# Performance work log

Hardware: AMD Instinct MI355X
Metric: run time of the kernel (lower is better)

The kernel has to match this reference:

```python
import jax, jax.numpy as jnp
import numpy as np

B, Z_DIM, T_DIM, ACT_E, CF, N_ACT, STEPS = 256, 256, 512, 256, 1024, 64, 64


def setup_inputs() -> dict:
    key = jax.random.key(0)
    ks = jax.random.split(key, 12)
    s = 0.02
    def n(k, shape):
        return jax.random.normal(k, shape, jnp.float32) * s
    return {
        "z": jax.random.normal(ks[0], (B, Z_DIM), jnp.float32),
        "W_z2t": n(ks[1], (T_DIM, Z_DIM)), "b_z2t": jnp.zeros((T_DIM,), jnp.float32),
        "E": n(ks[2], (N_ACT, ACT_E)),  # encoder_act2e embedding table
        "Wih_a": n(ks[3], (4 * CF, T_DIM + ACT_E)), "Whh_a": n(ks[4], (4 * CF, CF)),
        "bih_a": jnp.zeros((4 * CF,), jnp.float32), "bhh_a": jnp.zeros((4 * CF,), jnp.float32),
        "Wih_t": n(ks[5], (4 * CF, T_DIM + ACT_E + 1)), "Whh_t": n(ks[6], (4 * CF, CF)),
        "bih_t": jnp.zeros((4 * CF,), jnp.float32), "bhh_t": jnp.zeros((4 * CF,), jnp.float32),
        "W_act": n(ks[7], (N_ACT, CF)), "b_act": jnp.zeros((N_ACT,), jnp.float32),
        "W_ts1": n(ks[8], (CF // 2, CF)), "b_ts1": jnp.zeros((CF // 2,), jnp.float32),
        "W_ts2": n(ks[9], (1, CF // 2)), "b_ts2": jnp.zeros((1,), jnp.float32),
    }


def _lstm_step(x, h, c, Wih, Whh, bih, bhh):
    # PyTorch LSTM gate order: i, f, g, o
    gates = x @ Wih.T + h @ Whh.T + bih + bhh
    i, f, g, o = jnp.split(gates, 4, axis=-1)
    c = jax.nn.sigmoid(f) * c + jax.nn.sigmoid(i) * jnp.tanh(g)
    h = jax.nn.sigmoid(o) * jnp.tanh(c)
    return h, c


def reference(z, W_z2t, b_z2t, E, Wih_a, Whh_a, bih_a, bhh_a,
              Wih_t, Whh_t, bih_t, bhh_t, W_act, b_act,
              W_ts1, b_ts1, W_ts2, b_ts2):
    Bz = z.shape[0]
    t_rec = jax.nn.relu(z @ W_z2t.T + b_z2t)                 # [B, t_dim]
    zeros_h = jnp.zeros((Bz, CF), z.dtype)
    act_emb0 = jnp.broadcast_to(E[-1], (Bz, ACT_E))          # EOT token embedding
    ts0 = jnp.zeros((Bz, 1), z.dtype)

    def step(carry, _):
        h_a, c_a, h_t, c_t, act_emb, ts = carry
        x_a = jnp.concatenate([t_rec, act_emb], axis=1)       # [B, t_dim+act_e]
        h_a, c_a = _lstm_step(x_a, h_a, c_a, Wih_a, Whh_a, bih_a, bhh_a)
        logits = h_a @ W_act.T + b_act                        # [B, num_activities]
        act_emb = E[jnp.argmax(logits, axis=1)]               # [B, act_e]
        x_t = jnp.concatenate([t_rec, act_emb, ts], axis=1)   # [B, t_dim+act_e+1]
        h_t, c_t = _lstm_step(x_t, h_t, c_t, Wih_t, Whh_t, bih_t, bhh_t)
        ts = jax.nn.relu(h_t @ W_ts1.T + b_ts1) @ W_ts2.T + b_ts2  # [B, 1]
        return (h_a, c_a, h_t, c_t, act_emb, ts), (logits, ts)

    carry0 = (zeros_h, zeros_h, zeros_h, zeros_h, act_emb0, ts0)
    _, (logits_seq, ts_seq) = jax.lax.scan(step, carry0, None, length=STEPS)
    acts_rec = jax.nn.softmax(jnp.transpose(logits_seq, (1, 0, 2)), axis=2)  # [B, T, A]
    ts_rec = jnp.transpose(ts_seq[..., 0], (1, 0))                            # [B, T]
    return acts_rec, ts_rec
```

## Files before the change

### kernel.cpp

```cpp
#include <hip/hip_runtime.h>
#include <stdint.h>

typedef unsigned int u32;
typedef float  f32x4 __attribute__((ext_vector_type(4)));
typedef float  f32x2 __attribute__((ext_vector_type(2)));
typedef double f64x2 __attribute__((ext_vector_type(2)));
typedef double f64x4 __attribute__((ext_vector_type(4)));

constexpr int NT = 256;
constexpr int BB = 256;
constexpr int ZD = 256;
constexpr int TD = 512;
constexpr int CF = 1024;
constexpr int G4 = 4096;
constexpr int NA = 64;
constexpr int NSTEP = 64;
constexpr int TS_OFF = BB * NSTEP * NA;

constexpr int RSF = 34;

struct P {
  const float *z, *W_z2t, *b_z2t, *E, *Wih_a, *Whh_a, *bih_a, *bhh_a,
              *Wih_t, *Whh_t, *bih_t, *bhh_t, *W_act, *b_act, *W_ts1, *b_ts1, *W_ts2, *b_ts2;
  float* out;
  double *t_rec64, *pre_a64, *E_proj_a64, *h_a64, *c_a64, *gacc_a;
  float *t_rec32, *pre_t, *E_proj_t, *colt, *h_t, *c_t, *gacc_t, *ts_accum;
  int* idxb;
};

__device__ __forceinline__ float sigf(float x){ return 1.f / (1.f + expf(-x)); }
__device__ __forceinline__ float tanhf_(float x){
  float ax = fabsf(x); float e = expf(-2.f * ax);
  float t = 1.f - 2.f * e / (1.f + e);
  return x < 0.f ? -t : t;
}
__device__ __forceinline__ double sigd(double x){ return 1.0 / (1.0 + exp(-x)); }

__global__ void __launch_bounds__(NT) k_setup(P p){
  __shared__ double sz[ZD];
  const int bid = blockIdx.x, tid = threadIdx.x;
  for (int i = tid; i < ZD; i += NT) sz[i] = (double)p.z[bid * ZD + i];
  __syncthreads();
  for (int k = tid; k < TD; k += NT){
    const float* wr = p.W_z2t + (size_t)k * ZD;
    double a = 0.0;
    for (int j = 0; j < ZD; ++j) a = fma((double)wr[j], sz[j], a);
    a += (double)p.b_z2t[k];
    double t = a > 0.0 ? a : 0.0;
    p.t_rec64[(size_t)bid * TD + k] = t;
    p.t_rec32[(size_t)bid * TD + k] = (float)t;
  }
  for (int i = tid; i < CF; i += NT){
    p.c_a64[(size_t)bid * CF + i] = 0.0;
    p.h_a64[(size_t)bid * CF + i] = 0.0;
    p.c_t[(size_t)bid * CF + i] = 0.f;
    p.h_t[(size_t)bid * CF + i] = 0.f;
  }
  if (tid == 0){ p.idxb[bid] = NA - 1; p.ts_accum[bid] = 0.f; }
}

__global__ void __launch_bounds__(NT) k_eproj(P p){
  __shared__ double sz[ZD];
  const int bid = blockIdx.x, tid = threadIdx.x;
  if (bid < 256){
    const int erow = bid >> 2, cchunk = bid & 3;
    for (int i = tid; i < ZD; i += NT) sz[i] = (double)p.E[erow * ZD + i];
    __syncthreads();
    for (int ci = 0; ci < 4; ++ci){
      const int c = cchunk * 1024 + ci * 256 + tid;
      const float* wr = p.Wih_a + (size_t)c * 768 + 512;
      double a = 0.0;
      for (int j = 0; j < 256; ++j) a = fma((double)wr[j], sz[j], a);
      p.E_proj_a64[(size_t)erow * G4 + c] = a;
    }
  } else if (bid < 512){
    const int erow = (bid - 256) >> 2, cchunk = (bid - 256) & 3;
    for (int i = tid; i < ZD; i += NT) sz[i] = (double)p.E[erow * ZD + i];
    __syncthreads();
    for (int ci = 0; ci < 4; ++ci){
      const int c = cchunk * 1024 + ci * 256 + tid;
      const float* wr = p.Wih_t + (size_t)c * 769 + 512;
      float a = 0.f;
      for (int j = 0; j < 256; ++j) a = fmaf(wr[j], (float)sz[j], a);
      p.E_proj_t[(size_t)erow * G4 + c] = a;
    }
  } else {
    const int c = (bid - 512) * 256 + tid;
    p.colt[c] = p.Wih_t[(size_t)c * 769 + 768];
  }
}

template <bool A64, bool OUT64, bool BIAS>
__device__ void mgemm64(char* smem, const void* __restrict__ Av, int lda,
                        const float* __restrict__ B, int ldb,
                        int rowb, int colb, int K,
                        const void* __restrict__ addin,
                        const float* __restrict__ bih, const float* __restrict__ bhh,
                        void* __restrict__ outv){
  double* As = (double*)smem;
  double* Bs = As + 64 * RSF;
  const int tid = threadIdx.x;
  const int lane = tid & 63;
  const int wm = (tid >> 7) & 1, wn = (tid >> 6) & 1;
  const int m = lane & 15, q = lane >> 4;
  const int tr = tid >> 2, tkq = tid & 3;
  const double* A64p = (const double*)Av;
  const float*  A32p = (const float*)Av;

  double av[8], bv[8];
  auto loadchunk = [&](int kb){
    if (A64){
      const double* ap = A64p + (size_t)(rowb + tr) * lda + kb + tkq * 8;
      #pragma unroll
      for (int j = 0; j < 8; ++j) av[j] = ap[j];
    } else {
      const float* ap = A32p + (size_t)(rowb + tr) * lda + kb + tkq * 8;
      #pragma unroll
      for (int j = 0; j < 8; ++j) av[j] = (double)ap[j];
    }
    const float* bp = B + (size_t)(colb + tr) * ldb + kb + tkq * 8;
    #pragma unroll
    for (int j = 0; j < 8; ++j) bv[j] = (double)bp[j];
  };
  f64x4 acc[2][2];
  #pragma unroll
  for (int g = 0; g < 2; ++g)
    #pragma unroll
    for (int h = 0; h < 2; ++h) acc[g][h] = f64x4{0.0,0.0,0.0,0.0};

  loadchunk(0);
  for (int kb = 0; kb < K; kb += 32){
    __syncthreads();
    {
      double* arow = As + tr * RSF + tkq * 8;
      double* brow = Bs + tr * RSF + tkq * 8;
      #pragma unroll
      for (int j = 0; j < 4; ++j){
        *(f64x2*)(arow + j * 2) = f64x2{av[j], av[j + 4]};
        *(f64x2*)(brow + j * 2) = f64x2{bv[j], bv[j + 4]};
      }
    }
    __syncthreads();
    if (kb + 32 < K) loadchunk(kb + 32);
    #pragma unroll
    for (int sp = 0; sp < 4; ++sp){
      const f64x2 a0 = *(const f64x2*)(As + (wm * 32 +  0 + m) * RSF + sp * 8 + q * 2);
      const f64x2 a1 = *(const f64x2*)(As + (wm * 32 + 16 + m) * RSF + sp * 8 + q * 2);
      const f64x2 b0 = *(const f64x2*)(Bs + (wn * 32 +  0 + m) * RSF + sp * 8 + q * 2);
      const f64x2 b1 = *(const f64x2*)(Bs + (wn * 32 + 16 + m) * RSF + sp * 8 + q * 2);
      acc[0][0] = __builtin_amdgcn_mfma_f64_16x16x4f64(a0[0], b0[0], acc[0][0], 0, 0, 0);
      acc[0][1] = __builtin_amdgcn_mfma_f64_16x16x4f64(a0[0], b1[0], acc[0][1], 0, 0, 0);
      acc[1][0] = __builtin_amdgcn_mfma_f64_16x16x4f64(a1[0], b0[0], acc[1][0], 0, 0, 0);
      acc[1][1] = __builtin_amdgcn_mfma_f64_16x16x4f64(a1[0], b1[0], acc[1][1], 0, 0, 0);
      acc[0][0] = __builtin_amdgcn_mfma_f64_16x16x4f64(a0[1], b0[1], acc[0][0], 0, 0, 0);
      acc[0][1] = __builtin_amdgcn_mfma_f64_16x16x4f64(a0[1], b1[1], acc[0][1], 0, 0, 0);
      acc[1][0] = __builtin_amdgcn_mfma_f64_16x16x4f64(a1[1], b0[1], acc[1][0], 0, 0, 0);
      acc[1][1] = __builtin_amdgcn_mfma_f64_16x16x4f64(a1[1], b1[1], acc[1][1], 0, 0, 0);
    }
  }
  #pragma unroll
  for (int g = 0; g < 2; ++g){
    const int rb = rowb + wm * 32 + g * 16 + q;
    #pragma unroll
    for (int h = 0; h < 2; ++h){
      const int cc = colb + wn * 32 + h * 16 + m;
      if (BIAS){
        const double bb = (double)bih[cc] + (double)bhh[cc];
        #pragma unroll
        for (int v = 0; v < 4; ++v){
          if (OUT64) ((double*)outv)[(size_t)(rb + 4 * v) * G4 + cc] = acc[g][h][v] + bb;
          else       ((float*) outv)[(size_t)(rb + 4 * v) * G4 + cc] = (float)(acc[g][h][v] + bb);
        }
      } else {
        #pragma unroll
        for (int v = 0; v < 4; ++v){
          const size_t o = (size_t)(rb + 4 * v) * G4 + cc;
          if (OUT64) ((double*)outv)[o] = acc[g][h][v] + ((const double*)addin)[o];
          else       ((float*) outv)[o] = (float)(acc[g][h][v] + (double)((const float*)addin)[o]);
        }
      }
    }
  }
}

__device__ void tshead_j(const P& p, int bid, int hbuf){
  const int tid = threadIdx.x;
  const int tm = bid >> 6, tjq = bid & 63;
  const int rowb = tm * 32;
  const int rt = tid >> 3, j8 = tid & 7;
  const int j = tjq * 8 + j8;
  const float* __restrict__ hr = p.h_t + (size_t)hbuf * BB * CF + (size_t)(rowb + rt) * CF;
  const float* __restrict__ wr = p.W_ts1 + (size_t)j * CF;
  float a0=0,a1=0,a2=0,a3=0;
  for (int k = 0; k < CF; k += 16){
    f32x4 h0 = *(const f32x4*)(hr + k),     h1 = *(const f32x4*)(hr + k + 4);
    f32x4 h2 = *(const f32x4*)(hr + k + 8), h3 = *(const f32x4*)(hr + k + 12);
    f32x4 w0 = *(const f32x4*)(wr + k),     w1 = *(const f32x4*)(wr + k + 4);
    f32x4 w2 = *(const f32x4*)(wr + k + 8), w3 = *(const f32x4*)(wr + k + 12);
    a0 = fmaf(h0[0],w0[0], fmaf(h0[1],w0[1], fmaf(h0[2],w0[2], fmaf(h0[3],w0[3], a0))));
    a1 = fmaf(h1[0],w1[0], fmaf(h1[1],w1[1], fmaf(h1[2],w1[2], fmaf(h1[3],w1[3], a1))));
    a2 = fmaf(h2[0],w2[0], fmaf(h2[1],w2[1], fmaf(h2[2],w2[2], fmaf(h2[3],w2[3], a2))));
    a3 = fmaf(h3[0],w3[0], fmaf(h3[1],w3[1], fmaf(h3[2],w3[2], fmaf(h3[3],w3[3], a3))));
  }
  float v = ((a0 + a1) + (a2 + a3)) + p.b_ts1[j];
  v = (v > 0.f ? v : 0.f) * p.W_ts2[j];
  v += __shfl_xor(v, 1, 64);
  v += __shfl_xor(v, 2, 64);
  v += __shfl_xor(v, 4, 64);
  if (j8 == 0) atomicAdd(p.ts_accum + rowb + rt, v);
}

__global__ void __launch_bounds__(NT) k_pre(P p){
  __shared__ __align__(16) char smem[34816];
  const int bid = blockIdx.x;
  const int hsel = bid >> 8, sub = bid & 255;
  const int rowb = (sub >> 6) * 64, colb = (sub & 63) * 64;
  if (hsel == 0)
    mgemm64<true, true, true>(smem, p.t_rec64, TD, p.Wih_a, 768, rowb, colb, TD,
                              nullptr, p.bih_a, p.bhh_a, p.pre_a64);
  else
    mgemm64<false, false, true>(smem, p.t_rec32, TD, p.Wih_t, 769, rowb, colb, TD,
                                nullptr, p.bih_t, p.bhh_t, p.pre_t);
}

__global__ void __launch_bounds__(NT) k_stepA(P p, int s){
  __shared__ __align__(16) char smem[34816];
  const int bid = blockIdx.x;
  if (s > 0) tshead_j(p, bid, s & 1);
  const int hsel = bid >> 8, sub = bid & 255;
  const int rowb = (sub >> 6) * 64, colb = (sub & 63) * 64;
  const int rd = s & 1;
  if (hsel == 0)
    mgemm64<true, true, false>(smem, p.h_a64 + (size_t)rd * BB * CF, CF, p.Whh_a, CF,
                               rowb, colb, CF, p.pre_a64, nullptr, nullptr, p.gacc_a);
  else
    mgemm64<false, false, false>(smem, p.h_t + (size_t)rd * BB * CF, CF, p.Whh_t, CF,
                                 rowb, colb, CF, p.pre_t, nullptr, nullptr, p.gacc_t);
}

__global__ void __launch_bounds__(NT) k_stepB(P p, int s){
  __shared__ double shd[1092];
  const int b = blockIdx.x, tid = threadIdx.x;
  const int cur = (s + 1) & 1;
  int idxp = p.idxb[b];
  idxp = idxp < 0 ? 0 : (idxp > 63 ? 63 : idxp);
  {
    const double* ga = p.gacc_a + (size_t)b * G4;
    const double* ea = p.E_proj_a64 + (size_t)idxp * G4;
    const int c0 = tid * 4;
    #pragma unroll
    for (int jj = 0; jj < 4; ++jj){
      const int c = c0 + jj;
      double gi = ga[0*CF + c] + ea[0*CF + c];
      double gf = ga[1*CF + c] + ea[1*CF + c];
      double gg = ga[2*CF + c] + ea[2*CF + c];
      double go = ga[3*CF + c] + ea[3*CF + c];
      double cv = p.c_a64[(size_t)b * CF + c];
      double cn = sigd(gf) * cv + sigd(gi) * tanh(gg);
      double hn = sigd(go) * tanh(cn);
      p.c_a64[(size_t)b * CF + c] = cn;
      p.h_a64[(size_t)cur * BB * CF + (size_t)b * CF + c] = hn;
      shd[c] = hn;
    }
  }
  if (tid == 0) shd[1088] = (s == 0) ? 0.0 : ((double)p.ts_accum[b] + (double)p.b_ts2[0]);
  __syncthreads();
  {
    const int w = tid >> 6, l = tid & 63, l15 = l & 15, quad = l >> 4;
    const int a = w * 16 + l15;
    const float* wr = p.W_act + (size_t)a * CF + quad * 256;
    const double* hp = shd + quad * 256;
    double acc = 0.0;
    for (int kk = 0; kk < 256; kk += 4){
      acc = fma((double)wr[kk+0], hp[kk+0], acc);
      acc = fma((double)wr[kk+1], hp[kk+1], acc);
      acc = fma((double)wr[kk+2], hp[kk+2], acc);
      acc = fma((double)wr[kk+3], hp[kk+3], acc);
    }
    acc += __shfl_xor(acc, 16, 64);
    acc += __shfl_xor(acc, 32, 64);
    if (quad == 0) shd[1024 + a] = acc;
  }
  __syncthreads();
  if (tid < 64){
    double acc = shd[1024 + tid] + (double)p.b_act[tid];
    double m = acc;
    #pragma unroll
    for (int off = 32; off; off >>= 1) m = fmax(m, __shfl_xor(m, off, 64));
    unsigned long long ball = __ballot(acc == m);
    int idxv = __ffsll(ball) - 1;
    idxv = idxv < 0 ? 0 : (idxv > 63 ? 63 : idxv);
    double e = exp(acc - m);
    double ssum = e;
    #pragma unroll
    for (int off = 32; off; off >>= 1) ssum += __shfl_xor(ssum, off, 64);
    p.out[(size_t)b * (NSTEP * NA) + s * NA + tid] = (float)(e / ssum);
    if (tid == 0){
      p.idxb[b] = idxv;
      shd[1089] = (double)idxv;
      if (s > 0) p.out[TS_OFF + b * NSTEP + (s - 1)] = (float)shd[1088];
    }
  }
  __syncthreads();
  const float ts_val = (float)shd[1088];
  const int idxv = (int)shd[1089];
  const int c0 = tid * 4;
  const float* gb = p.gacc_t   + (size_t)b * G4;
  const float* eb = p.E_proj_t + (size_t)idxv * G4;
  f32x4 gi = *(const f32x4*)(gb + 0*CF + c0) + *(const f32x4*)(eb + 0*CF + c0) + ts_val * *(const f32x4*)(p.colt + 0*CF + c0);
  f32x4 gf = *(const f32x4*)(gb + 1*CF + c0) + *(const f32x4*)(eb + 1*CF + c0) + ts_val * *(const f32x4*)(p.colt + 1*CF + c0);
  f32x4 gg = *(const f32x4*)(gb + 2*CF + c0) + *(const f32x4*)(eb + 2*CF + c0) + ts_val * *(const f32x4*)(p.colt + 2*CF + c0);
  f32x4 go = *(const f32x4*)(gb + 3*CF + c0) + *(const f32x4*)(eb + 3*CF + c0) + ts_val * *(const f32x4*)(p.colt + 3*CF + c0);
  f32x4 cv = *(f32x4*)(p.c_t + (size_t)b * CF + c0);
  f32x4 cn, hn;
  #pragma unroll
  for (int jj = 0; jj < 4; ++jj){
    float cj = sigf(gf[jj]) * cv[jj] + sigf(gi[jj]) * tanhf_(gg[jj]);
    float hj = sigf(go[jj]) * tanhf_(cj);
    cn[jj] = cj; hn[jj] = hj;
  }
  *(f32x4*)(p.c_t + (size_t)b * CF + c0) = cn;
  *(f32x4*)(p.h_t + (size_t)cur * BB * CF + (size_t)b * CF + c0) = hn;
  __syncthreads();
  if (tid == 0) p.ts_accum[b] = 0.f;
}

__global__ void __launch_bounds__(NT) k_tsfin(P p){
  tshead_j(p, blockIdx.x, 0);
}
__global__ void __launch_bounds__(NT) k_tswrite(P p){
  p.out[TS_OFF + threadIdx.x * NSTEP + 63] = p.ts_accum[threadIdx.x] + p.b_ts2[0];
}

extern "C" void kernel_launch(void* const* d_in, const int* in_sizes, int n_in,
                              void* d_out, int out_size, void* d_ws, size_t ws_size,
                              hipStream_t stream){
  (void)in_sizes; (void)n_in; (void)out_size; (void)ws_size;
  P p;
  p.z     = (const float*)d_in[0];  p.W_z2t = (const float*)d_in[1];  p.b_z2t = (const float*)d_in[2];
  p.E     = (const float*)d_in[3];  p.Wih_a = (const float*)d_in[4];  p.Whh_a = (const float*)d_in[5];
  p.bih_a = (const float*)d_in[6];  p.bhh_a = (const float*)d_in[7];  p.Wih_t = (const float*)d_in[8];
  p.Whh_t = (const float*)d_in[9];  p.bih_t = (const float*)d_in[10]; p.bhh_t = (const float*)d_in[11];
  p.W_act = (const float*)d_in[12]; p.b_act = (const float*)d_in[13]; p.W_ts1 = (const float*)d_in[14];
  p.b_ts1 = (const float*)d_in[15]; p.W_ts2 = (const float*)d_in[16]; p.b_ts2 = (const float*)d_in[17];
  p.out = (float*)d_out;
  char* w = (char*)d_ws;
  size_t off = 0;
  auto alloc = [&](size_t bytes) -> void* { void* r = w + off; off += (bytes + 255) & ~(size_t)255; return r; };
  p.t_rec64    = (double*)alloc((size_t)BB * TD * 8);
  p.pre_a64    = (double*)alloc((size_t)BB * G4 * 8);
  p.E_proj_a64 = (double*)alloc((size_t)NA * G4 * 8);
  p.h_a64      = (double*)alloc((size_t)2 * BB * CF * 8);
  p.c_a64      = (double*)alloc((size_t)BB * CF * 8);
  p.gacc_a     = (double*)alloc((size_t)BB * G4 * 8);
  p.t_rec32    = (float*)alloc((size_t)BB * TD * 4);
  p.pre_t      = (float*)alloc((size_t)BB * G4 * 4);
  p.E_proj_t   = (float*)alloc((size_t)NA * G4 * 4);
  p.colt       = (float*)alloc((size_t)G4 * 4);
  p.h_t        = (float*)alloc((size_t)2 * BB * CF * 4);
  p.c_t        = (float*)alloc((size_t)BB * CF * 4);
  p.gacc_t     = (float*)alloc((size_t)BB * G4 * 4);
  p.ts_accum   = (float*)alloc((size_t)BB * 4);
  p.idxb       = (int*)  alloc((size_t)BB * 4);

  k_setup<<<dim3(256), dim3(NT), 0, stream>>>(p);
  k_eproj<<<dim3(528), dim3(NT), 0, stream>>>(p);
  k_pre  <<<dim3(512), dim3(NT), 0, stream>>>(p);
  for (int s = 0; s < NSTEP; ++s){
    k_stepA<<<dim3(512), dim3(NT), 0, stream>>>(p, s);
    k_stepB<<<dim3(256), dim3(NT), 0, stream>>>(p, s);
  }
  k_tsfin  <<<dim3(512), dim3(NT), 0, stream>>>(p);
  k_tswrite<<<dim3(1),   dim3(NT), 0, stream>>>(p);
}
```

Before: 11.73 ms.

## Double-buffer LDS tiles in f64 MFMA GEMM and stage B operand as fp32

The GEMM mainloop now uses two LDS buffers, so the next chunk can be staged while the current one is consumed. This needs only one barrier per K-chunk instead of two. The B operand is kept as fp32 in LDS and widened to double right before each MFMA, which halves its LDS footprint and store traffic. Row paddings change to odd strides (35 doubles, 33 floats) to spread accesses across LDS banks. Total LDS per block grows, which may cut the number of resident blocks per CU. The odd A stride also leaves the vector LDS accesses only 8-byte aligned.

```diff
diff --git a/kernel.cpp b/kernel.cpp
--- a/kernel.cpp
+++ b/kernel.cpp
@@ -17,7 +17,12 @@
 constexpr int NSTEP = 64;
 constexpr int TS_OFF = BB * NSTEP * NA;
 
-constexpr int RSF = 34;
+constexpr int RSA  = 35;
+constexpr int RBD  = 33;
+constexpr int ATILE = 64 * RSA * 8;
+constexpr int BTILE = 64 * RBD * 4;
+constexpr int BUFB  = ATILE + BTILE;
+constexpr int SMEMB = 2 * BUFB;
 
 struct P {
   const float *z, *W_z2t, *b_z2t, *E, *Wih_a, *Whh_a, *bih_a, *bhh_a,
@@ -97,8 +102,6 @@
                         const void* __restrict__ addin,
                         const float* __restrict__ bih, const float* __restrict__ bhh,
                         void* __restrict__ outv){
-  double* As = (double*)smem;
-  double* Bs = As + 64 * RSF;
   const int tid = threadIdx.x;
   const int lane = tid & 63;
   const int wm = (tid >> 7) & 1, wn = (tid >> 6) & 1;
@@ -107,7 +110,7 @@
   const double* A64p = (const double*)Av;
   const float*  A32p = (const float*)Av;
 
-  double av[8], bv[8];
+  double av[8]; float bvf[8];
   auto loadchunk = [&](int kb){
     if (A64){
       const double* ap = A64p + (size_t)(rowb + tr) * lda + kb + tkq * 8;
@@ -120,8 +123,18 @@
     }
     const float* bp = B + (size_t)(colb + tr) * ldb + kb + tkq * 8;
     #pragma unroll
-    for (int j = 0; j < 8; ++j) bv[j] = (double)bp[j];
+    for (int j = 0; j < 8; ++j) bvf[j] = bp[j];
   };
+  auto stage = [&](int buf){
+    double* arow = (double*)(smem + buf * BUFB) + tr * RSA + tkq * 8;
+    float*  brow = (float*)(smem + buf * BUFB + ATILE) + tr * RBD + tkq * 8;
+    #pragma unroll
+    for (int j = 0; j < 4; ++j){
+      *(f64x2*)(arow + j * 2) = f64x2{av[j], av[j + 4]};
+      *(f32x2*)(brow + j * 2) = f32x2{bvf[j], bvf[j + 4]};
+    }
+  };
+
   f64x4 acc[2][2];
   #pragma unroll
   for (int g = 0; g < 2; ++g)
@@ -129,33 +142,35 @@
     for (int h = 0; h < 2; ++h) acc[g][h] = f64x4{0.0,0.0,0.0,0.0};
 
   loadchunk(0);
-  for (int kb = 0; kb < K; kb += 32){
-    __syncthreads();
-    {
-      double* arow = As + tr * RSF + tkq * 8;
-      double* brow = Bs + tr * RSF + tkq * 8;
-      #pragma unroll
-      for (int j = 0; j < 4; ++j){
-        *(f64x2*)(arow + j * 2) = f64x2{av[j], av[j + 4]};
-        *(f64x2*)(brow + j * 2) = f64x2{bv[j], bv[j + 4]};
-      }
-    }
-    __syncthreads();
-    if (kb + 32 < K) loadchunk(kb + 32);
+  stage(0);
+  __syncthreads();
+  const int NCH = K >> 5;
+  for (int ch = 0; ch < NCH; ++ch){
+    const int cur = ch & 1;
+    const bool more = (ch + 1) < NCH;
+    if (more) loadchunk((ch + 1) << 5);
+    const double* As = (const double*)(smem + cur * BUFB);
+    const float*  Bs = (const float*)(smem + cur * BUFB + ATILE);
     #pragma unroll
     for (int sp = 0; sp < 4; ++sp){
-      const f64x2 a0 = *(const f64x2*)(As + (wm * 32 +  0 + m) * RSF + sp * 8 + q * 2);
-      const f64x2 a1 = *(const f64x2*)(As + (wm * 32 + 16 + m) * RSF + sp * 8 + q * 2);
-      const f64x2 b0 = *(const f64x2*)(Bs + (wn * 32 +  0 + m) * RSF + sp * 8 + q * 2);
-      const f64x2 b1 = *(const f64x2*)(Bs + (wn * 32 + 16 + m) * RSF + sp * 8 + q * 2);
-      acc[0][0] = __builtin_amdgcn_mfma_f64_16x16x4f64(a0[0], b0[0], acc[0][0], 0, 0, 0);
-      acc[0][1] = __builtin_amdgcn_mfma_f64_16x16x4f64(a0[0], b1[0], acc[0][1], 0, 0, 0);
-      acc[1][0] = __builtin_amdgcn_mfma_f64_16x16x4f64(a1[0], b0[0], acc[1][0], 0, 0, 0);
-      acc[1][1] = __builtin_amdgcn_mfma_f64_16x16x4f64(a1[0], b1[0], acc[1][1], 0, 0, 0);
-      acc[0][0] = __builtin_amdgcn_mfma_f64_16x16x4f64(a0[1], b0[1], acc[0][0], 0, 0, 0);
-      acc[0][1] = __builtin_amdgcn_mfma_f64_16x16x4f64(a0[1], b1[1], acc[0][1], 0, 0, 0);
-      acc[1][0] = __builtin_amdgcn_mfma_f64_16x16x4f64(a1[1], b0[1], acc[1][0], 0, 0, 0);
-      acc[1][1] = __builtin_amdgcn_mfma_f64_16x16x4f64(a1[1], b1[1], acc[1][1], 0, 0, 0);
+      const f64x2 a0 = *(const f64x2*)(As + (wm * 32 +  0 + m) * RSA + sp * 8 + q * 2);
+      const f64x2 a1 = *(const f64x2*)(As + (wm * 32 + 16 + m) * RSA + sp * 8 + q * 2);
+      const f32x2 b0f = *(const f32x2*)(Bs + (wn * 32 +  0 + m) * RBD + sp * 8 + q * 2);
+      const f32x2 b1f = *(const f32x2*)(Bs + (wn * 32 + 16 + m) * RBD + sp * 8 + q * 2);
+      const double b00 = (double)b0f[0], b04 = (double)b0f[1];
+      const double b10 = (double)b1f[0], b14 = (double)b1f[1];
+      acc[0][0] = __builtin_amdgcn_mfma_f64_16x16x4f64(a0[0], b00, acc[0][0], 0, 0, 0);
+      acc[0][1] = __builtin_amdgcn_mfma_f64_16x16x4f64(a0[0], b10, acc[0][1], 0, 0, 0);
+      acc[1][0] = __builtin_amdgcn_mfma_f64_16x16x4f64(a1[0], b00, acc[1][0], 0, 0, 0);
+      acc[1][1] = __builtin_amdgcn_mfma_f64_16x16x4f64(a1[0], b10, acc[1][1], 0, 0, 0);
+      acc[0][0] = __builtin_amdgcn_mfma_f64_16x16x4f64(a0[1], b04, acc[0][0], 0, 0, 0);
+      acc[0][1] = __builtin_amdgcn_mfma_f64_16x16x4f64(a0[1], b14, acc[0][1], 0, 0, 0);
+      acc[1][0] = __builtin_amdgcn_mfma_f64_16x16x4f64(a1[1], b04, acc[1][0], 0, 0, 0);
+      acc[1][1] = __builtin_amdgcn_mfma_f64_16x16x4f64(a1[1], b14, acc[1][1], 0, 0, 0);
+    }
+    if (more){
+      stage(cur ^ 1);
+      __syncthreads();
     }
   }
   #pragma unroll
@@ -211,7 +226,7 @@
 }
 
 __global__ void __launch_bounds__(NT) k_pre(P p){
-  __shared__ __align__(16) char smem[34816];
+  __shared__ __align__(16) char smem[SMEMB];
   const int bid = blockIdx.x;
   const int hsel = bid >> 8, sub = bid & 255;
   const int rowb = (sub >> 6) * 64, colb = (sub & 63) * 64;
@@ -224,7 +239,7 @@
 }
 
 __global__ void __launch_bounds__(NT) k_stepA(P p, int s){
-  __shared__ __align__(16) char smem[34816];
+  __shared__ __align__(16) char smem[SMEMB];
   const int bid = blockIdx.x;
   if (s > 0) tshead_j(p, bid, s & 1);
   const int hsel = bid >> 8, sub = bid & 255;
```

Measured after the change: 18.49 ms. 1.58x slower.

## Split recurrent GEMM K dimension across two block sets to double parallelism

Applied to the files above, without the earlier changes.

The per-step recurrent h@Whh GEMMs are split along K into two halves, each written to its own partial-sum buffer, and k_stepA launches 1024 blocks instead of 512. The gate kernel then adds the two partials. This is meant to raise occupancy across the GPU's compute units for the latency-bound per-step GEMM. The cost is extra global traffic for the second partial buffer and a slightly different summation order. The LDS row stride also changes from 34 to 35, presumably to change the bank-conflict pattern.

```diff
diff --git a/kernel.cpp b/kernel.cpp
--- a/kernel.cpp
+++ b/kernel.cpp
@@ -17,14 +17,16 @@
 constexpr int NSTEP = 64;
 constexpr int TS_OFF = BB * NSTEP * NA;
 
-constexpr int RSF = 34;
+constexpr int RSA   = 35;
+constexpr int ATILE = 64 * RSA * 8;
+constexpr int SMEMB = 2 * ATILE;
 
 struct P {
   const float *z, *W_z2t, *b_z2t, *E, *Wih_a, *Whh_a, *bih_a, *bhh_a,
               *Wih_t, *Whh_t, *bih_t, *bhh_t, *W_act, *b_act, *W_ts1, *b_ts1, *W_ts2, *b_ts2;
   float* out;
-  double *t_rec64, *pre_a64, *E_proj_a64, *h_a64, *c_a64, *gacc_a;
-  float *t_rec32, *pre_t, *E_proj_t, *colt, *h_t, *c_t, *gacc_t, *ts_accum;
+  double *t_rec64, *pre_a64, *E_proj_a64, *h_a64, *c_a64, *gacc_a, *gacc_a2;
+  float *t_rec32, *pre_t, *E_proj_t, *colt, *h_t, *c_t, *gacc_t, *gacc_t2, *ts_accum;
   int* idxb;
 };
 
@@ -90,15 +92,15 @@
   }
 }
 
-template <bool A64, bool OUT64, bool BIAS>
+template <bool A64, bool OUT64, int MODE>
 __device__ void mgemm64(char* smem, const void* __restrict__ Av, int lda,
                         const float* __restrict__ B, int ldb,
-                        int rowb, int colb, int K,
+                        int rowb, int colb, int kbase, int K,
                         const void* __restrict__ addin,
                         const float* __restrict__ bih, const float* __restrict__ bhh,
                         void* __restrict__ outv){
   double* As = (double*)smem;
-  double* Bs = As + 64 * RSF;
+  double* Bs = As + 64 * RSA;
   const int tid = threadIdx.x;
   const int lane = tid & 63;
   const int wm = (tid >> 7) & 1, wn = (tid >> 6) & 1;
@@ -110,15 +112,15 @@
   double av[8], bv[8];
   auto loadchunk = [&](int kb){
     if (A64){
-      const double* ap = A64p + (size_t)(rowb + tr) * lda + kb + tkq * 8;
+      const double* ap = A64p + (size_t)(rowb + tr) * lda + kbase + kb + tkq * 8;
       #pragma unroll
       for (int j = 0; j < 8; ++j) av[j] = ap[j];
     } else {
-      const float* ap = A32p + (size_t)(rowb + tr) * lda + kb + tkq * 8;
+      const float* ap = A32p + (size_t)(rowb + tr) * lda + kbase + kb + tkq * 8;
       #pragma unroll
       for (int j = 0; j < 8; ++j) av[j] = (double)ap[j];
     }
-    const float* bp = B + (size_t)(colb + tr) * ldb + kb + tkq * 8;
+    const float* bp = B + (size_t)(colb + tr) * ldb + kbase + kb + tkq * 8;
     #pragma unroll
     for (int j = 0; j < 8; ++j) bv[j] = (double)bp[j];
   };
@@ -132,8 +134,8 @@
   for (int kb = 0; kb < K; kb += 32){
     __syncthreads();
     {
-      double* arow = As + tr * RSF + tkq * 8;
-      double* brow = Bs + tr * RSF + tkq * 8;
+      double* arow = As + tr * RSA + tkq * 8;
+      double* brow = Bs + tr * RSA + tkq * 8;
       #pragma unroll
       for (int j = 0; j < 4; ++j){
         *(f64x2*)(arow + j * 2) = f64x2{av[j], av[j + 4]};
@@ -144,10 +146,10 @@
     if (kb + 32 < K) loadchunk(kb + 32);
     #pragma unroll
     for (int sp = 0; sp < 4; ++sp){
-      const f64x2 a0 = *(const f64x2*)(As + (wm * 32 +  0 + m) * RSF + sp * 8 + q * 2);
-      const f64x2 a1 = *(const f64x2*)(As + (wm * 32 + 16 + m) * RSF + sp * 8 + q * 2);
-      const f64x2 b0 = *(const f64x2*)(Bs + (wn * 32 +  0 + m) * RSF + sp * 8 + q * 2);
-      const f64x2 b1 = *(const f64x2*)(Bs + (wn * 32 + 16 + m) * RSF + sp * 8 + q * 2);
+      const f64x2 a0 = *(const f64x2*)(As + (wm * 32 +  0 + m) * RSA + sp * 8 + q * 2);
+      const f64x2 a1 = *(const f64x2*)(As + (wm * 32 + 16 + m) * RSA + sp * 8 + q * 2);
+      const f64x2 b0 = *(const f64x2*)(Bs + (wn * 32 +  0 + m) * RSA + sp * 8 + q * 2);
+      const f64x2 b1 = *(const f64x2*)(Bs + (wn * 32 + 16 + m) * RSA + sp * 8 + q * 2);
       acc[0][0] = __builtin_amdgcn_mfma_f64_16x16x4f64(a0[0], b0[0], acc[0][0], 0, 0, 0);
       acc[0][1] = __builtin_amdgcn_mfma_f64_16x16x4f64(a0[0], b1[0], acc[0][1], 0, 0, 0);
       acc[1][0] = __builtin_amdgcn_mfma_f64_16x16x4f64(a1[0], b0[0], acc[1][0], 0, 0, 0);
@@ -164,19 +166,26 @@
     #pragma unroll
     for (int h = 0; h < 2; ++h){
       const int cc = colb + wn * 32 + h * 16 + m;
-      if (BIAS){
+      if (MODE == 0){
         const double bb = (double)bih[cc] + (double)bhh[cc];
         #pragma unroll
         for (int v = 0; v < 4; ++v){
           if (OUT64) ((double*)outv)[(size_t)(rb + 4 * v) * G4 + cc] = acc[g][h][v] + bb;
           else       ((float*) outv)[(size_t)(rb + 4 * v) * G4 + cc] = (float)(acc[g][h][v] + bb);
         }
-      } else {
+      } else if (MODE == 1){
         #pragma unroll
         for (int v = 0; v < 4; ++v){
           const size_t o = (size_t)(rb + 4 * v) * G4 + cc;
           if (OUT64) ((double*)outv)[o] = acc[g][h][v] + ((const double*)addin)[o];
           else       ((float*) outv)[o] = (float)(acc[g][h][v] + (double)((const float*)addin)[o]);
+        }
+      } else {
+        #pragma unroll
+        for (int v = 0; v < 4; ++v){
+          const size_t o = (size_t)(rb + 4 * v) * G4 + cc;
+          if (OUT64) ((double*)outv)[o] = acc[g][h][v];
+          else       ((float*) outv)[o] = (float)acc[g][h][v];
         }
       }
     }
@@ -211,31 +220,42 @@
 }
 
 __global__ void __launch_bounds__(NT) k_pre(P p){
-  __shared__ __align__(16) char smem[34816];
+  __shared__ __align__(16) char smem[SMEMB];
   const int bid = blockIdx.x;
   const int hsel = bid >> 8, sub = bid & 255;
   const int rowb = (sub >> 6) * 64, colb = (sub & 63) * 64;
   if (hsel == 0)
-    mgemm64<true, true, true>(smem, p.t_rec64, TD, p.Wih_a, 768, rowb, colb, TD,
-                              nullptr, p.bih_a, p.bhh_a, p.pre_a64);
+    mgemm64<true, true, 0>(smem, p.t_rec64, TD, p.Wih_a, 768, rowb, colb, 0, TD,
+                           nullptr, p.bih_a, p.bhh_a, p.pre_a64);
   else
-    mgemm64<false, false, true>(smem, p.t_rec32, TD, p.Wih_t, 769, rowb, colb, TD,
-                                nullptr, p.bih_t, p.bhh_t, p.pre_t);
+    mgemm64<false, false, 0>(smem, p.t_rec32, TD, p.Wih_t, 769, rowb, colb, 0, TD,
+                             nullptr, p.bih_t, p.bhh_t, p.pre_t);
 }
 
 __global__ void __launch_bounds__(NT) k_stepA(P p, int s){
-  __shared__ __align__(16) char smem[34816];
+  __shared__ __align__(16) char smem[SMEMB];
   const int bid = blockIdx.x;
-  if (s > 0) tshead_j(p, bid, s & 1);
-  const int hsel = bid >> 8, sub = bid & 255;
+  if (s > 0 && bid < 512) tshead_j(p, bid, s & 1);
+  const int sub = bid & 255;
+  const int hsel = (bid >> 8) & 1, kh = (bid >> 9) & 1;
   const int rowb = (sub >> 6) * 64, colb = (sub & 63) * 64;
   const int rd = s & 1;
-  if (hsel == 0)
-    mgemm64<true, true, false>(smem, p.h_a64 + (size_t)rd * BB * CF, CF, p.Whh_a, CF,
-                               rowb, colb, CF, p.pre_a64, nullptr, nullptr, p.gacc_a);
-  else
-    mgemm64<false, false, false>(smem, p.h_t + (size_t)rd * BB * CF, CF, p.Whh_t, CF,
-                                 rowb, colb, CF, p.pre_t, nullptr, nullptr, p.gacc_t);
+  const int kbase = kh * 512;
+  if (hsel == 0){
+    if (kh == 0)
+      mgemm64<true, true, 1>(smem, p.h_a64 + (size_t)rd * BB * CF, CF, p.Whh_a, CF,
+                             rowb, colb, kbase, 512, p.pre_a64, nullptr, nullptr, p.gacc_a);
+    else
+      mgemm64<true, true, 2>(smem, p.h_a64 + (size_t)rd * BB * CF, CF, p.Whh_a, CF,
+                             rowb, colb, kbase, 512, nullptr, nullptr, nullptr, p.gacc_a2);
+  } else {
+    if (kh == 0)
+      mgemm64<false, false, 1>(smem, p.h_t + (size_t)rd * BB * CF, CF, p.Whh_t, CF,
+                               rowb, colb, kbase, 512, p.pre_t, nullptr, nullptr, p.gacc_t);
+    else
+      mgemm64<false, false, 2>(smem, p.h_t + (size_t)rd * BB * CF, CF, p.Whh_t, CF,
+                               rowb, colb, kbase, 512, nullptr, nullptr, nullptr, p.gacc_t2);
+  }
 }
 
 __global__ void __launch_bounds__(NT) k_stepB(P p, int s){
@@ -245,16 +265,17 @@
   int idxp = p.idxb[b];
   idxp = idxp < 0 ? 0 : (idxp > 63 ? 63 : idxp);
   {
-    const double* ga = p.gacc_a + (size_t)b * G4;
-    const double* ea = p.E_proj_a64 + (size_t)idxp * G4;
+    const double* ga  = p.gacc_a  + (size_t)b * G4;
+    const double* ga2 = p.gacc_a2 + (size_t)b * G4;
+    const double* ea  = p.E_proj_a64 + (size_t)idxp * G4;
     const int c0 = tid * 4;
     #pragma unroll
     for (int jj = 0; jj < 4; ++jj){
       const int c = c0 + jj;
-      double gi = ga[0*CF + c] + ea[0*CF + c];
-      double gf = ga[1*CF + c] + ea[1*CF + c];
-      double gg = ga[2*CF + c] + ea[2*CF + c];
-      double go = ga[3*CF + c] + ea[3*CF + c];
+      double gi = (ga[0*CF + c] + ga2[0*CF + c]) + ea[0*CF + c];
+      double gf = (ga[1*CF + c] + ga2[1*CF + c]) + ea[1*CF + c];
+      double gg = (ga[2*CF + c] + ga2[2*CF + c]) + ea[2*CF + c];
+      double go = (ga[3*CF + c] + ga2[3*CF + c]) + ea[3*CF + c];
       double cv = p.c_a64[(size_t)b * CF + c];
       double cn = sigd(gf) * cv + sigd(gi) * tanh(gg);
       double hn = sigd(go) * tanh(cn);
@@ -305,12 +326,13 @@
   const float ts_val = (float)shd[1088];
   const int idxv = (int)shd[1089];
   const int c0 = tid * 4;
-  const float* gb = p.gacc_t   + (size_t)b * G4;
-  const float* eb = p.E_proj_t + (size_t)idxv * G4;
-  f32x4 gi = *(const f32x4*)(gb + 0*CF + c0) + *(const f32x4*)(eb + 0*CF + c0) + ts_val * *(const f32x4*)(p.colt + 0*CF + c0);
-  f32x4 gf = *(const f32x4*)(gb + 1*CF + c0) + *(const f32x4*)(eb + 1*CF + c0) + ts_val * *(const f32x4*)(p.colt + 1*CF + c0);
-  f32x4 gg = *(const f32x4*)(gb + 2*CF + c0) + *(const f32x4*)(eb + 2*CF + c0) + ts_val * *(const f32x4*)(p.colt + 2*CF + c0);
-  f32x4 go = *(const f32x4*)(gb + 3*CF + c0) + *(const f32x4*)(eb + 3*CF + c0) + ts_val * *(const f32x4*)(p.colt + 3*CF + c0);
+  const float* gb  = p.gacc_t  + (size_t)b * G4;
+  const float* gb2 = p.gacc_t2 + (size_t)b * G4;
+  const float* eb  = p.E_proj_t + (size_t)idxv * G4;
+  f32x4 gi = (*(const f32x4*)(gb + 0*CF + c0) + *(const f32x4*)(gb2 + 0*CF + c0)) + *(const f32x4*)(eb + 0*CF + c0) + ts_val * *(const f32x4*)(p.colt + 0*CF + c0);
+  f32x4 gf = (*(const f32x4*)(gb + 1*CF + c0) + *(const f32x4*)(gb2 + 1*CF + c0)) + *(const f32x4*)(eb + 1*CF + c0) + ts_val * *(const f32x4*)(p.colt + 1*CF + c0);
+  f32x4 gg = (*(const f32x4*)(gb + 2*CF + c0) + *(const f32x4*)(gb2 + 2*CF + c0)) + *(const f32x4*)(eb + 2*CF + c0) + ts_val * *(const f32x4*)(p.colt + 2*CF + c0);
+  f32x4 go = (*(const f32x4*)(gb + 3*CF + c0) + *(const f32x4*)(gb2 + 3*CF + c0)) + *(const f32x4*)(eb + 3*CF + c0) + ts_val * *(const f32x4*)(p.colt + 3*CF + c0);
   f32x4 cv = *(f32x4*)(p.c_t + (size_t)b * CF + c0);
   f32x4 cn, hn;
   #pragma unroll
@@ -353,6 +375,7 @@
   p.h_a64      = (double*)alloc((size_t)2 * BB * CF * 8);
   p.c_a64      = (double*)alloc((size_t)BB * CF * 8);
   p.gacc_a     = (double*)alloc((size_t)BB * G4 * 8);
+  p.gacc_a2    = (double*)alloc((size_t)BB * G4 * 8);
   p.t_rec32    = (float*)alloc((size_t)BB * TD * 4);
   p.pre_t      = (float*)alloc((size_t)BB * G4 * 4);
   p.E_proj_t   = (float*)alloc((size_t)NA * G4 * 4);
@@ -360,6 +383,7 @@
   p.h_t        = (float*)alloc((size_t)2 * BB * CF * 4);
   p.c_t        = (float*)alloc((size_t)BB * CF * 4);
   p.gacc_t     = (float*)alloc((size_t)BB * G4 * 4);
+  p.gacc_t2    = (float*)alloc((size_t)BB * G4 * 4);
   p.ts_accum   = (float*)alloc((size_t)BB * 4);
   p.idxb       = (int*)  alloc((size_t)BB * 4);
 
@@ -367,8 +391,8 @@
   k_eproj<<<dim3(528), dim3(NT), 0, stream>>>(p);
   k_pre  <<<dim3(512), dim3(NT), 0, stream>>>(p);
   for (int s = 0; s < NSTEP; ++s){
-    k_stepA<<<dim3(512), dim3(NT), 0, stream>>>(p, s);
-    k_stepB<<<dim3(256), dim3(NT), 0, stream>>>(p, s);
+    k_stepA<<<dim3(1024), dim3(NT), 0, stream>>>(p, s);
+    k_stepB<<<dim3(256),  dim3(NT), 0, stream>>>(p, s);
   }
   k_tsfin  <<<dim3(512), dim3(NT), 0, stream>>>(p);
   k_tswrite<<<dim3(1),   dim3(NT), 0, stream>>>(p);
```

Measured after the change: 13.52 ms. 15.3% more time.

## Double-buffer LDS in recurrent step GEMM with explicit waitcnt software pipelining

Applied to the files above, without the earlier changes.

Replaces the single-buffered per-step recurrent GEMM with a double-buffered variant. Global loads for the next two K-chunks are issued ahead, and manual vmcnt/lgkmcnt waits plus raw barriers let MFMA on one LDS buffer overlap with staging into the other. B tiles are now held in LDS as fp32 instead of fp64, and row strides change to 35 and 33 to alter bank mapping. s_setprio is raised around the MFMA phases. The risks are higher LDS use per block, which can cut occupancy, and correctness depending on the hand-written waitcnt counts.

```diff
diff --git a/kernel.cpp b/kernel.cpp
--- a/kernel.cpp
+++ b/kernel.cpp
@@ -17,7 +17,12 @@
 constexpr int NSTEP = 64;
 constexpr int TS_OFF = BB * NSTEP * NA;
 
-constexpr int RSF = 34;
+constexpr int RSA   = 35;
+constexpr int RBD   = 33;
+constexpr int ATILE = 64 * RSA * 8;
+constexpr int BTILE = 64 * RBD * 4;
+constexpr int PSMEM = 2 * (ATILE + BTILE);
+constexpr int SSMEM = ATILE + 64 * RSA * 8;
 
 struct P {
   const float *z, *W_z2t, *b_z2t, *E, *Wih_a, *Whh_a, *bih_a, *bhh_a,
@@ -90,15 +95,14 @@
   }
 }
 
-template <bool A64, bool OUT64, bool BIAS>
-__device__ void mgemm64(char* smem, const void* __restrict__ Av, int lda,
-                        const float* __restrict__ B, int ldb,
-                        int rowb, int colb, int K,
-                        const void* __restrict__ addin,
-                        const float* __restrict__ bih, const float* __restrict__ bhh,
-                        void* __restrict__ outv){
+template <bool A64, bool OUT64>
+__device__ void mgemm64s(char* smem, const void* __restrict__ Av, int lda,
+                         const float* __restrict__ B, int ldb,
+                         int rowb, int colb, int K,
+                         const float* __restrict__ bih, const float* __restrict__ bhh,
+                         void* __restrict__ outv){
   double* As = (double*)smem;
-  double* Bs = As + 64 * RSF;
+  double* Bs = As + 64 * RSA;
   const int tid = threadIdx.x;
   const int lane = tid & 63;
   const int wm = (tid >> 7) & 1, wn = (tid >> 6) & 1;
@@ -132,8 +136,8 @@
   for (int kb = 0; kb < K; kb += 32){
     __syncthreads();
     {
-      double* arow = As + tr * RSF + tkq * 8;
-      double* brow = Bs + tr * RSF + tkq * 8;
+      double* arow = As + tr * RSA + tkq * 8;
+      double* brow = Bs + tr * RSA + tkq * 8;
       #pragma unroll
       for (int j = 0; j < 4; ++j){
         *(f64x2*)(arow + j * 2) = f64x2{av[j], av[j + 4]};
@@ -144,10 +148,10 @@
     if (kb + 32 < K) loadchunk(kb + 32);
     #pragma unroll
     for (int sp = 0; sp < 4; ++sp){
-      const f64x2 a0 = *(const f64x2*)(As + (wm * 32 +  0 + m) * RSF + sp * 8 + q * 2);
-      const f64x2 a1 = *(const f64x2*)(As + (wm * 32 + 16 + m) * RSF + sp * 8 + q * 2);
-      const f64x2 b0 = *(const f64x2*)(Bs + (wn * 32 +  0 + m) * RSF + sp * 8 + q * 2);
-      const f64x2 b1 = *(const f64x2*)(Bs + (wn * 32 + 16 + m) * RSF + sp * 8 + q * 2);
+      const f64x2 a0 = *(const f64x2*)(As + (wm * 32 +  0 + m) * RSA + sp * 8 + q * 2);
+      const f64x2 a1 = *(const f64x2*)(As + (wm * 32 + 16 + m) * RSA + sp * 8 + q * 2);
+      const f64x2 b0 = *(const f64x2*)(Bs + (wn * 32 +  0 + m) * RSA + sp * 8 + q * 2);
+      const f64x2 b1 = *(const f64x2*)(Bs + (wn * 32 + 16 + m) * RSA + sp * 8 + q * 2);
       acc[0][0] = __builtin_amdgcn_mfma_f64_16x16x4f64(a0[0], b0[0], acc[0][0], 0, 0, 0);
       acc[0][1] = __builtin_amdgcn_mfma_f64_16x16x4f64(a0[0], b1[0], acc[0][1], 0, 0, 0);
       acc[1][0] = __builtin_amdgcn_mfma_f64_16x16x4f64(a1[0], b0[0], acc[1][0], 0, 0, 0);
@@ -164,20 +168,136 @@
     #pragma unroll
     for (int h = 0; h < 2; ++h){
       const int cc = colb + wn * 32 + h * 16 + m;
-      if (BIAS){
-        const double bb = (double)bih[cc] + (double)bhh[cc];
-        #pragma unroll
-        for (int v = 0; v < 4; ++v){
-          if (OUT64) ((double*)outv)[(size_t)(rb + 4 * v) * G4 + cc] = acc[g][h][v] + bb;
-          else       ((float*) outv)[(size_t)(rb + 4 * v) * G4 + cc] = (float)(acc[g][h][v] + bb);
-        }
-      } else {
-        #pragma unroll
-        for (int v = 0; v < 4; ++v){
-          const size_t o = (size_t)(rb + 4 * v) * G4 + cc;
-          if (OUT64) ((double*)outv)[o] = acc[g][h][v] + ((const double*)addin)[o];
-          else       ((float*) outv)[o] = (float)(acc[g][h][v] + (double)((const float*)addin)[o]);
-        }
+      const double bb = (double)bih[cc] + (double)bhh[cc];
+      #pragma unroll
+      for (int v = 0; v < 4; ++v){
+        if (OUT64) ((double*)outv)[(size_t)(rb + 4 * v) * G4 + cc] = acc[g][h][v] + bb;
+        else       ((float*) outv)[(size_t)(rb + 4 * v) * G4 + cc] = (float)(acc[g][h][v] + bb);
+      }
+    }
+  }
+}
+
+template <bool A64, bool OUT64>
+__device__ void mgemm64p(char* smem, const void* __restrict__ Av, int lda,
+                         const float* __restrict__ B, int ldb,
+                         int rowb, int colb, int K,
+                         const void* __restrict__ addin, void* __restrict__ outv){
+  double* As0 = (double*)smem;
+  double* As1 = (double*)(smem + ATILE);
+  float*  Bs0 = (float*)(smem + 2 * ATILE);
+  float*  Bs1 = (float*)(smem + 2 * ATILE + BTILE);
+  const int tid = threadIdx.x, lane = tid & 63;
+  const int wm = (tid >> 7) & 1, wn = (tid >> 6) & 1;
+  const int m = lane & 15, q = lane >> 4;
+  const int tr = tid >> 2, tkq = tid & 3;
+  const double* A64p = (const double*)Av;
+  const float*  A32p = (const float*)Av;
+
+  f64x2 xA[4]; f32x4 xAf[2]; f32x4 xB[2];
+  f64x2 yA[4]; f32x4 yAf[2]; f32x4 yB[2];
+  f64x4 c00{0,0,0,0}, c01{0,0,0,0}, c10{0,0,0,0}, c11{0,0,0,0};
+
+#define ISSUE(kb, sA, sAf, sB) do{                                                      \
+    if (A64){                                                                           \
+      const f64x2* _ap = (const f64x2*)(A64p + (size_t)(rowb + tr) * lda + (kb) + tkq * 8); \
+      sA[0] = _ap[0]; sA[1] = _ap[1]; sA[2] = _ap[2]; sA[3] = _ap[3];                   \
+    } else {                                                                            \
+      const f32x4* _ap = (const f32x4*)(A32p + (size_t)(rowb + tr) * lda + (kb) + tkq * 8); \
+      sAf[0] = _ap[0]; sAf[1] = _ap[1];                                                 \
+    }                                                                                   \
+    const f32x4* _bp = (const f32x4*)(B + (size_t)(colb + tr) * ldb + (kb) + tkq * 8);  \
+    sB[0] = _bp[0]; sB[1] = _bp[1];                                                     \
+  }while(0)
+
+#define WAITV()  do{ if (A64) asm volatile("s_waitcnt vmcnt(6)" ::: "memory");          \
+                     else     asm volatile("s_waitcnt vmcnt(4)" ::: "memory"); }while(0)
+#define WAITV0() asm volatile("s_waitcnt vmcnt(0)" ::: "memory")
+#define LGKM0_BAR() do{ asm volatile("s_waitcnt lgkmcnt(0)" ::: "memory");              \
+                        __builtin_amdgcn_s_barrier(); }while(0)
+
+#define STAGEJ(_aw, _bw, sA, sAf, sB, j) do{                                            \
+    f64x2 _v;                                                                           \
+    if (A64) _v = f64x2{ sA[(j) >> 1][(j) & 1], sA[((j) >> 1) + 2][(j) & 1] };          \
+    else     _v = f64x2{ (double)sAf[0][(j)], (double)sAf[1][(j)] };                    \
+    *(f64x2*)((_aw) + (j) * 2) = _v;                                                    \
+    *(f32x2*)((_bw) + (j) * 2) = f32x2{ sB[0][(j)], sB[1][(j)] };                       \
+  }while(0)
+
+#define PHASE(bufsel, DOSTAGE, sA, sAf, sB) do{                                         \
+    const double* _As = (bufsel) ? As1 : As0;                                           \
+    const float*  _Bs = (bufsel) ? Bs1 : Bs0;                                           \
+    double* _aw = ((bufsel) ? As0 : As1) + tr * RSA + tkq * 8;                          \
+    float*  _bw = ((bufsel) ? Bs0 : Bs1) + tr * RBD + tkq * 8;                          \
+    __builtin_amdgcn_s_setprio(1);                                                      \
+    _Pragma("unroll")                                                                   \
+    for (int _sp = 0; _sp < 4; ++_sp){                                                  \
+      const f64x2 _a0 = *(const f64x2*)(_As + (wm * 32 +  0 + m) * RSA + _sp * 8 + q * 2); \
+      const f64x2 _a1 = *(const f64x2*)(_As + (wm * 32 + 16 + m) * RSA + _sp * 8 + q * 2); \
+      const f32x2 _b0 = *(const f32x2*)(_Bs + (wn * 32 +  0 + m) * RBD + _sp * 8 + q * 2); \
+      const f32x2 _b1 = *(const f32x2*)(_Bs + (wn * 32 + 16 + m) * RBD + _sp * 8 + q * 2); \
+      const double _b00 = (double)_b0[0], _b04 = (double)_b0[1];                        \
+      const double _b10 = (double)_b1[0], _b14 = (double)_b1[1];                        \
+      c00 = __builtin_amdgcn_mfma_f64_16x16x4f64(_a0[0], _b00, c00, 0, 0, 0);           \
+      c01 = __builtin_amdgcn_mfma_f64_16x16x4f64(_a0[0], _b10, c01, 0, 0, 0);           \
+      c10 = __builtin_amdgcn_mfma_f64_16x16x4f64(_a1[0], _b00, c10, 0, 0, 0);           \
+      c11 = __builtin_amdgcn_mfma_f64_16x16x4f64(_a1[0], _b10, c11, 0, 0, 0);           \
+      c00 = __builtin_amdgcn_mfma_f64_16x16x4f64(_a0[1], _b04, c00, 0, 0, 0);           \
+      c01 = __builtin_amdgcn_mfma_f64_16x16x4f64(_a0[1], _b14, c01, 0, 0, 0);           \
+      c10 = __builtin_amdgcn_mfma_f64_16x16x4f64(_a1[1], _b04, c10, 0, 0, 0);           \
+      c11 = __builtin_amdgcn_mfma_f64_16x16x4f64(_a1[1], _b14, c11, 0, 0, 0);           \
+      if (DOSTAGE) STAGEJ(_aw, _bw, sA, sAf, sB, _sp);                                  \
+    }                                                                                   \
+    __builtin_amdgcn_s_setprio(0);                                                      \
+  }while(0)
+
+  const int NCH = K >> 5;
+  ISSUE(0, yA, yAf, yB);
+  WAITV0();
+  {
+    double* aw = As0 + tr * RSA + tkq * 8;
+    float*  bw = Bs0 + tr * RBD + tkq * 8;
+    #pragma unroll
+    for (int j = 0; j < 4; ++j) STAGEJ(aw, bw, yA, yAf, yB, j);
+  }
+  ISSUE(32, xA, xAf, xB);
+  LGKM0_BAR();
+
+  int ch = 0;
+  for (; ch + 3 < NCH; ch += 2){
+    ISSUE((ch + 2) * 32, yA, yAf, yB);
+    WAITV();
+    PHASE(0, true, xA, xAf, xB);
+    LGKM0_BAR();
+    ISSUE((ch + 3) * 32, xA, xAf, xB);
+    WAITV();
+    PHASE(1, true, yA, yAf, yB);
+    LGKM0_BAR();
+  }
+  WAITV0();
+  PHASE(0, true, xA, xAf, xB);
+  LGKM0_BAR();
+  PHASE(1, false, xA, xAf, xB);
+
+#undef ISSUE
+#undef WAITV
+#undef WAITV0
+#undef LGKM0_BAR
+#undef STAGEJ
+#undef PHASE
+
+  #pragma unroll
+  for (int g = 0; g < 2; ++g){
+    const int rb = rowb + wm * 32 + g * 16 + q;
+    #pragma unroll
+    for (int h = 0; h < 2; ++h){
+      const f64x4 a = g ? (h ? c11 : c10) : (h ? c01 : c00);
+      const int cc = colb + wn * 32 + h * 16 + m;
+      #pragma unroll
+      for (int v = 0; v < 4; ++v){
+        const size_t o = (size_t)(rb + 4 * v) * G4 + cc;
+        if (OUT64) ((double*)outv)[o] = a[v] + ((const double*)addin)[o];
+        else       ((float*) outv)[o] = (float)(a[v] + (double)((const float*)addin)[o]);
       }
     }
   }
@@ -211,31 +331,31 @@
 }
 
 __global__ void __launch_bounds__(NT) k_pre(P p){
-  __shared__ __align__(16) char smem[34816];
+  __shared__ __align__(16) char smem[SSMEM];
   const int bid = blockIdx.x;
   const int hsel = bid >> 8, sub = bid & 255;
   const int rowb = (sub >> 6) * 64, colb = (sub & 63) * 64;
   if (hsel == 0)
-    mgemm64<true, true, true>(smem, p.t_rec64, TD, p.Wih_a, 768, rowb, colb, TD,
-                              nullptr, p.bih_a, p.bhh_a, p.pre_a64);
+    mgemm64s<true, true>(smem, p.t_rec64, TD, p.Wih_a, 768, rowb, colb, TD,
+                         p.bih_a, p.bhh_a, p.pre_a64);
   else
-    mgemm64<false, false, true>(smem, p.t_rec32, TD, p.Wih_t, 769, rowb, colb, TD,
-                                nullptr, p.bih_t, p.bhh_t, p.pre_t);
+    mgemm64s<false, false>(smem, p.t_rec32, TD, p.Wih_t, 769, rowb, colb, TD,
+                           p.bih_t, p.bhh_t, p.pre_t);
 }
 
 __global__ void __launch_bounds__(NT) k_stepA(P p, int s){
-  __shared__ __align__(16) char smem[34816];
+  __shared__ __align__(16) char smem[PSMEM];
   const int bid = blockIdx.x;
   if (s > 0) tshead_j(p, bid, s & 1);
   const int hsel = bid >> 8, sub = bid & 255;
   const int rowb = (sub >> 6) * 64, colb = (sub & 63) * 64;
   const int rd = s & 1;
   if (hsel == 0)
-    mgemm64<true, true, false>(smem, p.h_a64 + (size_t)rd * BB * CF, CF, p.Whh_a, CF,
-                               rowb, colb, CF, p.pre_a64, nullptr, nullptr, p.gacc_a);
+    mgemm64p<true, true>(smem, p.h_a64 + (size_t)rd * BB * CF, CF, p.Whh_a, CF,
+                         rowb, colb, CF, p.pre_a64, p.gacc_a);
   else
-    mgemm64<false, false, false>(smem, p.h_t + (size_t)rd * BB * CF, CF, p.Whh_t, CF,
-                                 rowb, colb, CF, p.pre_t, nullptr, nullptr, p.gacc_t);
+    mgemm64p<false, false>(smem, p.h_t + (size_t)rd * BB * CF, CF, p.Whh_t, CF,
+                           rowb, colb, CF, p.pre_t, p.gacc_t);
 }
 
 __global__ void __launch_bounds__(NT) k_stepB(P p, int s){
```

Measured after the change: 17.24 ms. 1.47x slower.
